# Kernel optimization log

Measured on AMD Instinct MI355X. Metric: run time of the kernel, lower is better.

## Reference

```python
import jax, jax.numpy as jnp
import numpy as np

N, E, D, H = 50000, 800000, 128, 64


def _norm_adj(edge_index, num_nodes):
    # add self loops, then w_ij = d_i^{-1/2} d_j^{-1/2} with deg = in-degree of col
    loops = jnp.arange(num_nodes)
    row = jnp.concatenate([edge_index[0], loops])
    col = jnp.concatenate([edge_index[1], loops])
    deg = jax.ops.segment_sum(jnp.ones_like(col, dtype=jnp.float32), col, num_segments=num_nodes)
    dinv = jnp.where(deg > 0, jax.lax.rsqrt(deg), 0.0)
    w = dinv[row] * dinv[col]
    return row, col, w


def _spmm(row, col, w, x, num_nodes):
    # y[row] += w * x[col]  (torch.sparse.mm(adj, x))
    return jax.ops.segment_sum(w[:, None] * x[col], row, num_segments=num_nodes)


def setup_inputs() -> dict:
    key = jax.random.key(0)
    ks = jax.random.split(key, 8)
    inp = {
        "x": jax.random.normal(ks[0], (N, D), dtype=jnp.float32),
        "edge_index": jax.random.randint(ks[1], (2, E), 0, N),
        "num_nodes": N,
    }
    # per-branch, per-layer Linear weights stored as [in, hid] (x @ W)
    wk = jax.random.split(ks[2], 6)
    s = 0.05
    inp["homo_W0"] = jax.random.normal(wk[0], (D, H), dtype=jnp.float32) * s
    inp["homo_W1"] = jax.random.normal(wk[1], (H, H), dtype=jnp.float32) * s
    inp["full_W0"] = jax.random.normal(wk[2], (D, H), dtype=jnp.float32) * s
    inp["full_W1"] = jax.random.normal(wk[3], (H, H), dtype=jnp.float32) * s
    inp["het_W0"] = jax.random.normal(wk[4], (D, H), dtype=jnp.float32) * s
    inp["het_W1"] = jax.random.normal(wk[5], (H, H), dtype=jnp.float32) * s
    for name in ("homo_a0", "homo_a1", "full_a0", "full_a1", "het_a0", "het_a1",
                 "w_homo", "w_full", "w_hetero"):
        inp[name] = jnp.float32(1.0)
    return inp


def reference(x, edge_index, num_nodes,
              homo_W0, homo_W1, full_W0, full_W1, het_W0, het_W1,
              homo_a0, homo_a1, full_a0, full_a1, het_a0, het_a1,
              w_homo, w_full, w_hetero):
    row, col, w = _norm_adj(edge_index, num_nodes)

    def homo_layer(h, W, a):
        return jax.nn.relu(a * (_spmm(row, col, w, h, num_nodes) @ W))

    def full_layer(h, W, a):
        return jax.nn.relu(a * (h @ W))

    def het_layer(h, W, a):
        # L = I - A  =>  L @ h = h - A @ h
        return jax.nn.relu(a * ((h - _spmm(row, col, w, h, num_nodes)) @ W))

    h_homo = homo_layer(homo_layer(x, homo_W0, homo_a0), homo_W1, homo_a1)
    h_full = full_layer(full_layer(x, full_W0, full_a0), full_W1, full_a1)
    h_het = het_layer(het_layer(x, het_W0, het_a0), het_W1, het_a1)
    combined = w_homo * h_homo + w_full * h_full + w_hetero * h_het
    return (combined, h_homo, h_full, h_het)
```

## Files before the change

### kernel.cpp

```cpp
#include <hip/hip_runtime.h>


typedef __attribute__((ext_vector_type(8))) short short8;
typedef __attribute__((ext_vector_type(4))) float f32x4;

static __device__ __forceinline__ unsigned short f2bf(float f) {
    unsigned int u = __float_as_uint(f);
    u += 0x7FFFu + ((u >> 16) & 1u);
    return (unsigned short)(u >> 16);
}
static __device__ __forceinline__ float bflo(unsigned int pv) {
    return __uint_as_float(pv << 16);
}
static __device__ __forceinline__ float bfhi(unsigned int pv) {
    return __uint_as_float(pv & 0xFFFF0000u);
}

#define PSHIFT 7
#define PSIZE  128
#define NPART_MAX 400
#define PCAP   3072
#define ACHUNK 6272

__global__ __launch_bounds__(256) void wpackT_kernel(
    const float* __restrict__ w10, const float* __restrict__ w11,
    const float* __restrict__ w12, const float* __restrict__ w20,
    const float* __restrict__ w21, const float* __restrict__ w22,
    unsigned short* __restrict__ out)
{
    const int i = blockIdx.x * 256 + threadIdx.x;
    const int L1 = 3 * 64 * 128;
    if (i < L1) {
        const int b = i >> 13, col = (i >> 7) & 63, k = i & 127;
        const float* __restrict__ w = (b == 0) ? w10 : ((b == 1) ? w11 : w12);
        out[i] = f2bf(w[k * 64 + col]);
    } else if (i < L1 + 3 * 64 * 64) {
        const int j = i - L1;
        const int b = j >> 12, col = (j >> 6) & 63, k = j & 63;
        const float* __restrict__ w = (b == 0) ? w20 : ((b == 1) ? w21 : w22);
        out[i] = f2bf(w[k * 64 + col]);
    }
}

__global__ __launch_bounds__(256) void radix_kernel(
    const int* __restrict__ ei, int E, int npart,
    int* __restrict__ gcnt_r, int* __restrict__ gcnt_c,
    unsigned int* __restrict__ rbuf, unsigned short* __restrict__ cbuf)
{
    __shared__ int hist_r[NPART_MAX], lofs_r[NPART_MAX], resv_r[NPART_MAX];
    __shared__ int hist_c[NPART_MAX], lofs_c[NPART_MAX], resv_c[NPART_MAX];
    __shared__ int seg_r[16], seg_c[16];
    __shared__ unsigned int   sr[ACHUNK];
    __shared__ unsigned short sc[ACHUNK];
    const int tid = threadIdx.x;
    const int e0 = blockIdx.x * ACHUNK;
    const int e1 = (e0 + ACHUNK < E) ? e0 + ACHUNK : E;
    const int cnt = e1 - e0;
    if (cnt <= 0) return;

    for (int i = tid; i < npart; i += 256) { hist_r[i] = 0; hist_c[i] = 0; }
    __syncthreads();

    for (int e = e0 + tid; e < e1; e += 256) {
        const int r = ei[e], c = ei[E + e];
        atomicAdd(&hist_r[r >> PSHIFT], 1);
        atomicAdd(&hist_c[c >> PSHIFT], 1);
    }
    __syncthreads();

    const int SEG = (npart + 7) / 8;
    if (tid < 8) {
        int s = 0;
        const int a = tid * SEG, b = (a + SEG < npart) ? a + SEG : npart;
        for (int i = a; i < b; ++i) { lofs_r[i] = s; s += hist_r[i]; }
        seg_r[tid] = s;
    } else if (tid >= 64 && tid < 72) {
        const int t = tid - 64;
        int s = 0;
        const int a = t * SEG, b = (a + SEG < npart) ? a + SEG : npart;
        for (int i = a; i < b; ++i) { lofs_c[i] = s; s += hist_c[i]; }
        seg_c[t] = s;
    }
    __syncthreads();
    if (tid == 0) {
        int s = 0;
        for (int k = 0; k < 8; ++k) { const int t = seg_r[k]; seg_r[k] = s; s += t; }
    } else if (tid == 64) {
        int s = 0;
        for (int k = 0; k < 8; ++k) { const int t = seg_c[k]; seg_c[k] = s; s += t; }
    }
    __syncthreads();
    for (int i = tid; i < npart; i += 256) {
        lofs_r[i] += seg_r[i / SEG];
        lofs_c[i] += seg_c[i / SEG];
    }
    __syncthreads();

    for (int i = tid; i < npart; i += 256) {
        resv_r[i] = atomicAdd(&gcnt_r[i], hist_r[i]);
        resv_c[i] = atomicAdd(&gcnt_c[i], hist_c[i]);
        hist_r[i] = 0; hist_c[i] = 0;
    }
    __syncthreads();

    for (int e = e0 + tid; e < e1; e += 256) {
        const int r = ei[e], c = ei[E + e];
        const int pr = r >> PSHIFT, pc = c >> PSHIFT;
        const int jr = lofs_r[pr] + atomicAdd(&hist_r[pr], 1);
        const int jc = lofs_c[pc] + atomicAdd(&hist_c[pc], 1);
        sr[jr] = ((unsigned int)r << 16) | (unsigned int)c;
        sc[jc] = (unsigned short)c;
    }
    __syncthreads();

    for (int j = tid; j < cnt; j += 256) {
        const unsigned int rc = sr[j];
        const int p = (int)(rc >> 16) >> PSHIFT;
        const int idx = resv_r[p] + (j - lofs_r[p]);
        if (idx < PCAP) rbuf[(size_t)p * PCAP + idx] = rc;
    }
    for (int j = tid; j < cnt; j += 256) {
        const unsigned short cv = sc[j];
        const int p = (int)cv >> PSHIFT;
        const int idx = resv_c[p] + (j - lofs_c[p]);
        if (idx < PCAP) cbuf[(size_t)p * PCAP + idx] = cv;
    }
}

__global__ __launch_bounds__(256) void bucket_kernel(
    const unsigned int* __restrict__ rbuf, const unsigned short* __restrict__ cbuf,
    const int* __restrict__ gcnt_r, const int* __restrict__ gcnt_c, int N,
    unsigned short* __restrict__ bucket, int* __restrict__ cur,
    float* __restrict__ dinv)
{
    __shared__ unsigned short sbucket[PSIZE * 64];
    __shared__ int scur[PSIZE], sdeg[PSIZE];
    const int tid = threadIdx.x;
    const int p = blockIdx.x;
    const int lo = p << PSHIFT;
    const int sl = (lo + PSIZE < N) ? PSIZE : N - lo;
    if (sl <= 0) return;

    for (int i = tid; i < sl; i += 256) { scur[i] = 0; sdeg[i] = 0; }
    __syncthreads();

    int cnt_r = gcnt_r[p]; if (cnt_r > PCAP) cnt_r = PCAP;
    int cnt_c = gcnt_c[p]; if (cnt_c > PCAP) cnt_c = PCAP;

    for (int e = tid; e < cnt_r; e += 256) {
        const unsigned int rc = rbuf[(size_t)p * PCAP + e];
        const int local = (int)(rc >> 16) - lo;
        const int pos = atomicAdd(&scur[local], 1);
        if (pos < 64) sbucket[local * 64 + pos] = (unsigned short)(rc & 0xFFFFu);
    }
    for (int e = tid; e < cnt_c; e += 256) {
        atomicAdd(&sdeg[(int)cbuf[(size_t)p * PCAP + e] - lo], 1);
    }
    __syncthreads();

    for (int i = tid; i < sl; i += 256) {
        cur[lo + i]  = scur[i];
        dinv[lo + i] = 1.0f / sqrtf((float)sdeg[i] + 1.0f);
    }
    unsigned int* gb = (unsigned int*)(bucket + (size_t)lo * 64);
    const unsigned int* sb = (const unsigned int*)sbucket;
    for (int i = tid; i < sl * 32; i += 256) gb[i] = sb[i];
}

__global__ __launch_bounds__(256) void gemm_l1_kernel(
    const float* __restrict__ x, const unsigned short* __restrict__ Wt,
    const float* __restrict__ dinv,
    unsigned short* __restrict__ Pb, unsigned short* __restrict__ full1b,
    const float* __restrict__ alphaF, int N)
{
    __shared__ __align__(16) unsigned short sx[64 * 136];
    const int tid = threadIdx.x;
    const int row0 = blockIdx.x * 64;

    #pragma unroll
    for (int j = 0; j < 8; ++j) {
        const int idx = j * 256 + tid;
        const int row = idx >> 5;
        const int c4  = idx & 31;
        float4 v = make_float4(0.f, 0.f, 0.f, 0.f);
        if (row0 + row < N) v = ((const float4*)x)[(size_t)(row0 + row) * 32 + c4];
        const unsigned int lo = (unsigned int)f2bf(v.x) | ((unsigned int)f2bf(v.y) << 16);
        const unsigned int hi = (unsigned int)f2bf(v.z) | ((unsigned int)f2bf(v.w) << 16);
        *(uint2*)&sx[row * 136 + c4 * 4] = make_uint2(lo, hi);
    }
    __syncthreads();

    const int lane = tid & 63;
    const int w = tid >> 6;
    const int g = lane >> 4;
    const int m = lane & 15;
    const float alpha = alphaF[0];

    short8 afr[4];
    #pragma unroll
    for (int kk = 0; kk < 4; ++kk)
        afr[kk] = *(const short8*)&sx[(16 * w + m) * 136 + kk * 32 + g * 8];

    const int rbase = row0 + 16 * w + g * 4;
    float dv[4];
    #pragma unroll
    for (int j = 0; j < 4; ++j)
        dv[j] = (rbase + j < N) ? dinv[rbase + j] : 0.f;

    #pragma unroll 1
    for (int b = 0; b < 3; ++b) {
        const unsigned short* __restrict__ Wb = Wt + b * 8192;
        f32x4 acc0 = {0.f, 0.f, 0.f, 0.f};
        f32x4 acc1 = {0.f, 0.f, 0.f, 0.f};
        f32x4 acc2 = {0.f, 0.f, 0.f, 0.f};
        f32x4 acc3 = {0.f, 0.f, 0.f, 0.f};
        #pragma unroll
        for (int kk = 0; kk < 4; ++kk) {
            const unsigned short* wk = Wb + m * 128 + kk * 32 + g * 8;
            const short8 b0 = *(const short8*)(wk);
            const short8 b1 = *(const short8*)(wk + 16 * 128);
            const short8 b2 = *(const short8*)(wk + 32 * 128);
            const short8 b3 = *(const short8*)(wk + 48 * 128);
            acc0 = __builtin_amdgcn_mfma_f32_16x16x32_bf16(afr[kk], b0, acc0, 0, 0, 0);
            acc1 = __builtin_amdgcn_mfma_f32_16x16x32_bf16(afr[kk], b1, acc1, 0, 0, 0);
            acc2 = __builtin_amdgcn_mfma_f32_16x16x32_bf16(afr[kk], b2, acc2, 0, 0, 0);
            acc3 = __builtin_amdgcn_mfma_f32_16x16x32_bf16(afr[kk], b3, acc3, 0, 0, 0);
        }
        #pragma unroll
        for (int j = 0; j < 4; ++j) {
            const int row = rbase + j;
            if (row < N) {
                if (b < 2) {
                    unsigned short* p = Pb + (size_t)row * 128 + b * 64 + m;
                    p[0]  = f2bf(dv[j] * acc0[j]);
                    p[16] = f2bf(dv[j] * acc1[j]);
                    p[32] = f2bf(dv[j] * acc2[j]);
                    p[48] = f2bf(dv[j] * acc3[j]);
                } else {
                    unsigned short* p = full1b + (size_t)row * 64 + m;
                    p[0]  = f2bf(fmaxf(alpha * acc0[j], 0.f));
                    p[16] = f2bf(fmaxf(alpha * acc1[j], 0.f));
                    p[32] = f2bf(fmaxf(alpha * acc2[j], 0.f));
                    p[48] = f2bf(fmaxf(alpha * acc3[j], 0.f));
                }
            }
        }
    }
}

__global__ __launch_bounds__(256) void gemm_l2_kernel(
    const unsigned short* __restrict__ h1b, const unsigned short* __restrict__ t1b,
    const unsigned short* __restrict__ f1b, const unsigned short* __restrict__ Wt2,
    const float* __restrict__ dinv,
    unsigned short* __restrict__ Qb, float* __restrict__ outF,
    const float* __restrict__ alphaF, int N)
{
    __shared__ __align__(16) unsigned short sx[3][64 * 72];
    const int tid = threadIdx.x;
    const int row0 = blockIdx.x * 64;

    #pragma unroll
    for (int b = 0; b < 3; ++b) {
        const unsigned short* __restrict__ in = (b == 0) ? h1b : ((b == 1) ? t1b : f1b);
        #pragma unroll
        for (int j = 0; j < 2; ++j) {
            const int idx = j * 256 + tid;
            const int row = idx >> 3, seg = idx & 7;
            uint4 v = make_uint4(0, 0, 0, 0);
            if (row0 + row < N) v = ((const uint4*)in)[(size_t)(row0 + row) * 8 + seg];
            *(uint4*)&sx[b][row * 72 + seg * 8] = v;
        }
    }
    __syncthreads();

    const int lane = tid & 63;
    const int w = tid >> 6;
    const int g = lane >> 4, m = lane & 15;
    const float alpha = alphaF[0];
    const int rbase = row0 + 16 * w + g * 4;

    float dv[4];
    #pragma unroll
    for (int j = 0; j < 4; ++j)
        dv[j] = (rbase + j < N) ? dinv[rbase + j] : 0.f;

    #pragma unroll 1
    for (int b = 0; b < 3; ++b) {
        const short8 afr0 = *(const short8*)&sx[b][(16 * w + m) * 72 + g * 8];
        const short8 afr1 = *(const short8*)&sx[b][(16 * w + m) * 72 + 32 + g * 8];
        const unsigned short* __restrict__ Wb = Wt2 + b * 4096;
        f32x4 acc0 = {0.f, 0.f, 0.f, 0.f};
        f32x4 acc1 = {0.f, 0.f, 0.f, 0.f};
        f32x4 acc2 = {0.f, 0.f, 0.f, 0.f};
        f32x4 acc3 = {0.f, 0.f, 0.f, 0.f};
        #pragma unroll
        for (int kk = 0; kk < 2; ++kk) {
            const short8 af = kk ? afr1 : afr0;
            const unsigned short* wk = Wb + m * 64 + kk * 32 + g * 8;
            const short8 b0 = *(const short8*)(wk);
            const short8 b1 = *(const short8*)(wk + 16 * 64);
            const short8 b2 = *(const short8*)(wk + 32 * 64);
            const short8 b3 = *(const short8*)(wk + 48 * 64);
            acc0 = __builtin_amdgcn_mfma_f32_16x16x32_bf16(af, b0, acc0, 0, 0, 0);
            acc1 = __builtin_amdgcn_mfma_f32_16x16x32_bf16(af, b1, acc1, 0, 0, 0);
            acc2 = __builtin_amdgcn_mfma_f32_16x16x32_bf16(af, b2, acc2, 0, 0, 0);
            acc3 = __builtin_amdgcn_mfma_f32_16x16x32_bf16(af, b3, acc3, 0, 0, 0);
        }
        #pragma unroll
        for (int j = 0; j < 4; ++j) {
            const int row = rbase + j;
            if (row < N) {
                if (b < 2) {
                    unsigned short* p = Qb + (size_t)row * 128 + b * 64 + m;
                    p[0]  = f2bf(dv[j] * acc0[j]);
                    p[16] = f2bf(dv[j] * acc1[j]);
                    p[32] = f2bf(dv[j] * acc2[j]);
                    p[48] = f2bf(dv[j] * acc3[j]);
                } else {
                    float* p = outF + (size_t)row * 64 + m;
                    p[0]  = fmaxf(alpha * acc0[j], 0.f);
                    p[16] = fmaxf(alpha * acc1[j], 0.f);
                    p[32] = fmaxf(alpha * acc2[j], 0.f);
                    p[48] = fmaxf(alpha * acc3[j], 0.f);
                }
            }
        }
    }
}

__global__ __launch_bounds__(256) void spmm1_kernel(
    const unsigned short* __restrict__ Pb, const unsigned short* __restrict__ bucket,
    const int* __restrict__ cnt, const float* __restrict__ dinv,
    unsigned short* __restrict__ homo1b, unsigned short* __restrict__ het1b,
    const float* __restrict__ aH, const float* __restrict__ aT, int N)
{
    const int i = blockIdx.x * 4 + (threadIdx.x >> 6);
    if (i >= N) return;
    const int lane = threadIdx.x & 63;
    const int g  = lane >> 4;
    const int fl = lane & 15;
    const uint4* __restrict__ P16 = (const uint4*)Pb;
    const float di = dinv[i];
    const uint4 us = P16[(size_t)i * 16 + fl];
    float ps[8];
    ps[0] = bflo(us.x); ps[1] = bfhi(us.x); ps[2] = bflo(us.y); ps[3] = bfhi(us.y);
    ps[4] = bflo(us.z); ps[5] = bfhi(us.z); ps[6] = bflo(us.w); ps[7] = bfhi(us.w);
    int n = cnt[i]; if (n > 64) n = 64;
    const unsigned int* __restrict__ bp = (const unsigned int*)(bucket + (size_t)i * 64);
    float acc[8];
    #pragma unroll
    for (int j = 0; j < 8; ++j) acc[j] = 0.f;

    for (int k0 = 0; k0 < n; k0 += 16) {
        const int wbase = (k0 >> 1) + (g >> 1);
        const unsigned int pw0 = bp[wbase];
        const unsigned int pw1 = bp[wbase + 2];
        const unsigned int pw2 = bp[wbase + 4];
        const unsigned int pw3 = bp[wbase + 6];
        const int k_0 = k0 + g, k_1 = k0 + 4 + g, k_2 = k0 + 8 + g, k_3 = k0 + 12 + g;
        const int c0 = (k_0 < n) ? (int)((g & 1) ? (pw0 >> 16) : (pw0 & 0xFFFFu)) : i;
        const int c1 = (k_1 < n) ? (int)((g & 1) ? (pw1 >> 16) : (pw1 & 0xFFFFu)) : i;
        const int c2 = (k_2 < n) ? (int)((g & 1) ? (pw2 >> 16) : (pw2 & 0xFFFFu)) : i;
        const int c3 = (k_3 < n) ? (int)((g & 1) ? (pw3 >> 16) : (pw3 & 0xFFFFu)) : i;
        const float s0 = (k_0 < n) ? 1.f : 0.f;
        const float s1 = (k_1 < n) ? 1.f : 0.f;
        const float s2 = (k_2 < n) ? 1.f : 0.f;
        const float s3 = (k_3 < n) ? 1.f : 0.f;
        const uint4 u0 = P16[(size_t)c0 * 16 + fl];
        const uint4 u1 = P16[(size_t)c1 * 16 + fl];
        const uint4 u2 = P16[(size_t)c2 * 16 + fl];
        const uint4 u3 = P16[(size_t)c3 * 16 + fl];
        acc[0] = fmaf(s0, bflo(u0.x), acc[0]); acc[1] = fmaf(s0, bfhi(u0.x), acc[1]);
        acc[2] = fmaf(s0, bflo(u0.y), acc[2]); acc[3] = fmaf(s0, bfhi(u0.y), acc[3]);
        acc[4] = fmaf(s0, bflo(u0.z), acc[4]); acc[5] = fmaf(s0, bfhi(u0.z), acc[5]);
        acc[6] = fmaf(s0, bflo(u0.w), acc[6]); acc[7] = fmaf(s0, bfhi(u0.w), acc[7]);
        acc[0] = fmaf(s1, bflo(u1.x), acc[0]); acc[1] = fmaf(s1, bfhi(u1.x), acc[1]);
        acc[2] = fmaf(s1, bflo(u1.y), acc[2]); acc[3] = fmaf(s1, bfhi(u1.y), acc[3]);
        acc[4] = fmaf(s1, bflo(u1.z), acc[4]); acc[5] = fmaf(s1, bfhi(u1.z), acc[5]);
        acc[6] = fmaf(s1, bflo(u1.w), acc[6]); acc[7] = fmaf(s1, bfhi(u1.w), acc[7]);
        acc[0] = fmaf(s2, bflo(u2.x), acc[0]); acc[1] = fmaf(s2, bfhi(u2.x), acc[1]);
        acc[2] = fmaf(s2, bflo(u2.y), acc[2]); acc[3] = fmaf(s2, bfhi(u2.y), acc[3]);
        acc[4] = fmaf(s2, bflo(u2.z), acc[4]); acc[5] = fmaf(s2, bfhi(u2.z), acc[5]);
        acc[6] = fmaf(s2, bflo(u2.w), acc[6]); acc[7] = fmaf(s2, bfhi(u2.w), acc[7]);
        acc[0] = fmaf(s3, bflo(u3.x), acc[0]); acc[1] = fmaf(s3, bfhi(u3.x), acc[1]);
        acc[2] = fmaf(s3, bflo(u3.y), acc[2]); acc[3] = fmaf(s3, bfhi(u3.y), acc[3]);
        acc[4] = fmaf(s3, bflo(u3.z), acc[4]); acc[5] = fmaf(s3, bfhi(u3.z), acc[5]);
        acc[6] = fmaf(s3, bflo(u3.w), acc[6]); acc[7] = fmaf(s3, bfhi(u3.w), acc[7]);
    }
    float y[8];
    #pragma unroll
    for (int j = 0; j < 8; ++j) {
        acc[j] += __shfl_xor(acc[j], 16);
        acc[j] += __shfl_xor(acc[j], 32);
        y[j] = di * (acc[j] + ps[j]);
    }
    if (lane < 8) {
        const float a = aH[0];
        uint4 o;
        o.x = (unsigned int)f2bf(fmaxf(a * y[0], 0.f)) |
              ((unsigned int)f2bf(fmaxf(a * y[1], 0.f)) << 16);
        o.y = (unsigned int)f2bf(fmaxf(a * y[2], 0.f)) |
              ((unsigned int)f2bf(fmaxf(a * y[3], 0.f)) << 16);
        o.z = (unsigned int)f2bf(fmaxf(a * y[4], 0.f)) |
              ((unsigned int)f2bf(fmaxf(a * y[5], 0.f)) << 16);
        o.w = (unsigned int)f2bf(fmaxf(a * y[6], 0.f)) |
              ((unsigned int)f2bf(fmaxf(a * y[7], 0.f)) << 16);
        ((uint4*)homo1b)[(size_t)i * 8 + lane] = o;
    } else if (lane < 16) {
        const float a = aT[0];
        const float rdi = 1.0f / di;
        float v[8];
        #pragma unroll
        for (int j = 0; j < 8; ++j) v[j] = fmaxf(a * (ps[j] * rdi - y[j]), 0.f);
        uint4 o;
        o.x = (unsigned int)f2bf(v[0]) | ((unsigned int)f2bf(v[1]) << 16);
        o.y = (unsigned int)f2bf(v[2]) | ((unsigned int)f2bf(v[3]) << 16);
        o.z = (unsigned int)f2bf(v[4]) | ((unsigned int)f2bf(v[5]) << 16);
        o.w = (unsigned int)f2bf(v[6]) | ((unsigned int)f2bf(v[7]) << 16);
        ((uint4*)het1b)[(size_t)i * 8 + (lane - 8)] = o;
    }
}

__global__ __launch_bounds__(256) void spmm2_kernel(
    const unsigned short* __restrict__ Qb, const unsigned short* __restrict__ bucket,
    const int* __restrict__ cnt, const float* __restrict__ dinv,
    const float* __restrict__ full2,
    float* __restrict__ outComb, float* __restrict__ outHomo, float* __restrict__ outHet,
    const float* __restrict__ aH, const float* __restrict__ aT,
    const float* __restrict__ wH, const float* __restrict__ wF, const float* __restrict__ wT,
    int N)
{
    const int i = blockIdx.x * 4 + (threadIdx.x >> 6);
    if (i >= N) return;
    const int lane = threadIdx.x & 63;
    const int g  = lane >> 4;
    const int fl = lane & 15;
    const uint4* __restrict__ Q16 = (const uint4*)Qb;
    const float di = dinv[i];
    const uint4 us = Q16[(size_t)i * 16 + fl];
    float ps[8];
    ps[0] = bflo(us.x); ps[1] = bfhi(us.x); ps[2] = bflo(us.y); ps[3] = bfhi(us.y);
    ps[4] = bflo(us.z); ps[5] = bfhi(us.z); ps[6] = bflo(us.w); ps[7] = bfhi(us.w);
    int n = cnt[i]; if (n > 64) n = 64;
    const unsigned int* __restrict__ bp = (const unsigned int*)(bucket + (size_t)i * 64);
    float acc[8];
    #pragma unroll
    for (int j = 0; j < 8; ++j) acc[j] = 0.f;

    for (int k0 = 0; k0 < n; k0 += 16) {
        const int wbase = (k0 >> 1) + (g >> 1);
        const unsigned int pw0 = bp[wbase];
        const unsigned int pw1 = bp[wbase + 2];
        const unsigned int pw2 = bp[wbase + 4];
        const unsigned int pw3 = bp[wbase + 6];
        const int k_0 = k0 + g, k_1 = k0 + 4 + g, k_2 = k0 + 8 + g, k_3 = k0 + 12 + g;
        const int c0 = (k_0 < n) ? (int)((g & 1) ? (pw0 >> 16) : (pw0 & 0xFFFFu)) : i;
        const int c1 = (k_1 < n) ? (int)((g & 1) ? (pw1 >> 16) : (pw1 & 0xFFFFu)) : i;
        const int c2 = (k_2 < n) ? (int)((g & 1) ? (pw2 >> 16) : (pw2 & 0xFFFFu)) : i;
        const int c3 = (k_3 < n) ? (int)((g & 1) ? (pw3 >> 16) : (pw3 & 0xFFFFu)) : i;
        const float s0 = (k_0 < n) ? 1.f : 0.f;
        const float s1 = (k_1 < n) ? 1.f : 0.f;
        const float s2 = (k_2 < n) ? 1.f : 0.f;
        const float s3 = (k_3 < n) ? 1.f : 0.f;
        const uint4 u0 = Q16[(size_t)c0 * 16 + fl];
        const uint4 u1 = Q16[(size_t)c1 * 16 + fl];
        const uint4 u2 = Q16[(size_t)c2 * 16 + fl];
        const uint4 u3 = Q16[(size_t)c3 * 16 + fl];
        acc[0] = fmaf(s0, bflo(u0.x), acc[0]); acc[1] = fmaf(s0, bfhi(u0.x), acc[1]);
        acc[2] = fmaf(s0, bflo(u0.y), acc[2]); acc[3] = fmaf(s0, bfhi(u0.y), acc[3]);
        acc[4] = fmaf(s0, bflo(u0.z), acc[4]); acc[5] = fmaf(s0, bfhi(u0.z), acc[5]);
        acc[6] = fmaf(s0, bflo(u0.w), acc[6]); acc[7] = fmaf(s0, bfhi(u0.w), acc[7]);
        acc[0] = fmaf(s1, bflo(u1.x), acc[0]); acc[1] = fmaf(s1, bfhi(u1.x), acc[1]);
        acc[2] = fmaf(s1, bflo(u1.y), acc[2]); acc[3] = fmaf(s1, bfhi(u1.y), acc[3]);
        acc[4] = fmaf(s1, bflo(u1.z), acc[4]); acc[5] = fmaf(s1, bfhi(u1.z), acc[5]);
        acc[6] = fmaf(s1, bflo(u1.w), acc[6]); acc[7] = fmaf(s1, bfhi(u1.w), acc[7]);
        acc[0] = fmaf(s2, bflo(u2.x), acc[0]); acc[1] = fmaf(s2, bfhi(u2.x), acc[1]);
        acc[2] = fmaf(s2, bflo(u2.y), acc[2]); acc[3] = fmaf(s2, bfhi(u2.y), acc[3]);
        acc[4] = fmaf(s2, bflo(u2.z), acc[4]); acc[5] = fmaf(s2, bfhi(u2.z), acc[5]);
        acc[6] = fmaf(s2, bflo(u2.w), acc[6]); acc[7] = fmaf(s2, bfhi(u2.w), acc[7]);
        acc[0] = fmaf(s3, bflo(u3.x), acc[0]); acc[1] = fmaf(s3, bfhi(u3.x), acc[1]);
        acc[2] = fmaf(s3, bflo(u3.y), acc[2]); acc[3] = fmaf(s3, bfhi(u3.y), acc[3]);
        acc[4] = fmaf(s3, bflo(u3.z), acc[4]); acc[5] = fmaf(s3, bfhi(u3.z), acc[5]);
        acc[6] = fmaf(s3, bflo(u3.w), acc[6]); acc[7] = fmaf(s3, bfhi(u3.w), acc[7]);
    }
    float y[8];
    #pragma unroll
    for (int j = 0; j < 8; ++j) {
        acc[j] += __shfl_xor(acc[j], 16);
        acc[j] += __shfl_xor(acc[j], 32);
        y[j] = di * (acc[j] + ps[j]);
    }
    float v[8];
    if (fl < 8) {
        const float a = aH[0];
        #pragma unroll
        for (int j = 0; j < 8; ++j) v[j] = fmaxf(a * y[j], 0.f);
    } else {
        const float a = aT[0];
        const float rdi = 1.0f / di;
        #pragma unroll
        for (int j = 0; j < 8; ++j) v[j] = fmaxf(a * (ps[j] * rdi - y[j]), 0.f);
    }
    if (lane < 8) {
        float4* dst = (float4*)(outHomo + (size_t)i * 64 + 8 * lane);
        dst[0] = make_float4(v[0], v[1], v[2], v[3]);
        dst[1] = make_float4(v[4], v[5], v[6], v[7]);
    } else if (lane < 16) {
        float4* dst = (float4*)(outHet + (size_t)i * 64 + 8 * (lane - 8));
        dst[0] = make_float4(v[0], v[1], v[2], v[3]);
        dst[1] = make_float4(v[4], v[5], v[6], v[7]);
    }
    float t[8];
    #pragma unroll
    for (int j = 0; j < 8; ++j) t[j] = __shfl_xor(v[j], 8);
    if (lane < 8) {
        const float4* f4 = (const float4*)(full2 + (size_t)i * 64 + 8 * lane);
        const float4 fa = f4[0], fb = f4[1];
        const float cwh = wH[0], cwf = wF[0], cwt = wT[0];
        float4* dst = (float4*)(outComb + (size_t)i * 64 + 8 * lane);
        dst[0] = make_float4(cwh * v[0] + cwf * fa.x + cwt * t[0],
                             cwh * v[1] + cwf * fa.y + cwt * t[1],
                             cwh * v[2] + cwf * fa.z + cwt * t[2],
                             cwh * v[3] + cwf * fa.w + cwt * t[3]);
        dst[1] = make_float4(cwh * v[4] + cwf * fb.x + cwt * t[4],
                             cwh * v[5] + cwf * fb.y + cwt * t[5],
                             cwh * v[6] + cwf * fb.z + cwt * t[6],
                             cwh * v[7] + cwf * fb.w + cwt * t[7]);
    }
}

extern "C" void kernel_launch(void* const* d_in, const int* in_sizes, int n_in,
                              void* d_out, int out_size, void* d_ws, size_t ws_size,
                              hipStream_t stream)
{
    const float* x  = (const float*)d_in[0];
    const int*   ei = (const int*)d_in[1];
    const int N = in_sizes[0] / 128;
    const int E = in_sizes[1] / 2;
    const float* homo_W0 = (const float*)d_in[3];
    const float* homo_W1 = (const float*)d_in[4];
    const float* full_W0 = (const float*)d_in[5];
    const float* full_W1 = (const float*)d_in[6];
    const float* het_W0  = (const float*)d_in[7];
    const float* het_W1  = (const float*)d_in[8];
    const float* homo_a0 = (const float*)d_in[9];
    const float* homo_a1 = (const float*)d_in[10];
    const float* full_a0 = (const float*)d_in[11];
    const float* full_a1 = (const float*)d_in[12];
    const float* het_a0  = (const float*)d_in[13];
    const float* het_a1  = (const float*)d_in[14];
    const float* w_homo  = (const float*)d_in[15];
    const float* w_full  = (const float*)d_in[16];
    const float* w_het   = (const float*)d_in[17];

    char* ws = (char*)d_ws;
    size_t off = 0;
    auto alloc = [&](size_t bytes) -> char* {
        char* p = ws + off;
        off = (off + bytes + 511) & ~(size_t)511;
        return p;
    };
    int*            cur    = (int*)alloc((size_t)N * 4);
    float*          dinv   = (float*)alloc((size_t)N * 4);
    unsigned short* bucket = (unsigned short*)alloc((size_t)N * 64 * 2);
    int*            gcnt   = (int*)alloc((size_t)2 * NPART_MAX * 4);
    unsigned short* Wt     = (unsigned short*)alloc((size_t)(3 * 64 * 128 + 3 * 64 * 64) * 2);
    const size_t rbuf_sz = (size_t)NPART_MAX * PCAP * 4;
    const size_t cbuf_sz = (size_t)NPART_MAX * PCAP * 2;
    size_t unionA_sz = (size_t)N * 128 * 2;
    if (rbuf_sz + cbuf_sz > unionA_sz) unionA_sz = rbuf_sz + cbuf_sz;
    char*           unionA = alloc(unionA_sz);
    unsigned int*   rbuf   = (unsigned int*)unionA;
    unsigned short* cbuf   = (unsigned short*)(unionA + rbuf_sz);
    unsigned short* Pb     = (unsigned short*)unionA;
    unsigned short* full1b = (unsigned short*)alloc((size_t)N * 64 * 2);
    unsigned short* homo1b = (unsigned short*)alloc((size_t)N * 64 * 2);
    unsigned short* het1b  = (unsigned short*)alloc((size_t)N * 64 * 2);
    unsigned short* Qb     = Pb;

    float* out      = (float*)d_out;
    float* outComb  = out;
    float* outHomo  = out + (size_t)N * 64;
    float* outFull  = out + (size_t)2 * N * 64;
    float* outHet   = out + (size_t)3 * N * 64;

    const int npart = (N + PSIZE - 1) >> PSHIFT;

    hipMemsetAsync(gcnt, 0, (size_t)2 * NPART_MAX * 4, stream);

    wpackT_kernel<<<(3 * 64 * 128 + 3 * 64 * 64 + 255) / 256, 256, 0, stream>>>(
        homo_W0, het_W0, full_W0, homo_W1, het_W1, full_W1, Wt);

    const int ablocks = (E + ACHUNK - 1) / ACHUNK;
    radix_kernel<<<ablocks, 256, 0, stream>>>(
        ei, E, npart, gcnt, gcnt + NPART_MAX, rbuf, cbuf);
    bucket_kernel<<<npart, 256, 0, stream>>>(
        rbuf, cbuf, gcnt, gcnt + NPART_MAX, N, bucket, cur, dinv);

    gemm_l1_kernel<<<(N + 63) / 64, 256, 0, stream>>>(
        x, Wt, dinv, Pb, full1b, full_a0, N);
    spmm1_kernel<<<(N + 3) / 4, 256, 0, stream>>>(
        Pb, bucket, cur, dinv, homo1b, het1b, homo_a0, het_a0, N);

    gemm_l2_kernel<<<(N + 63) / 64, 256, 0, stream>>>(
        homo1b, het1b, full1b, Wt + 3 * 64 * 128, dinv, Qb, outFull, full_a1, N);
    spmm2_kernel<<<(N + 3) / 4, 256, 0, stream>>>(
        Qb, bucket, cur, dinv, outFull, outComb, outHomo, outHet,
        homo_a1, het_a1, w_homo, w_full, w_het, N);
}
```

Measured before the change: 159.7 us.

## Split radix partitioning by side, fuse counter reset, vectorize bucket loads

```diff
diff --git a/kernel.cpp b/kernel.cpp
--- a/kernel.cpp
+++ b/kernel.cpp
@@ -20,15 +20,16 @@
 #define PSIZE  128
 #define NPART_MAX 400
 #define PCAP   3072
-#define ACHUNK 6272
-
-__global__ __launch_bounds__(256) void wpackT_kernel(
+#define ACHUNK 3136
+
+__global__ __launch_bounds__(256) void prep_kernel(
     const float* __restrict__ w10, const float* __restrict__ w11,
     const float* __restrict__ w12, const float* __restrict__ w20,
     const float* __restrict__ w21, const float* __restrict__ w22,
-    unsigned short* __restrict__ out)
+    unsigned short* __restrict__ out, int* __restrict__ gcnt)
 {
     const int i = blockIdx.x * 256 + threadIdx.x;
+    if (i < 2 * NPART_MAX) gcnt[i] = 0;
     const int L1 = 3 * 64 * 128;
     if (i < L1) {
         const int b = i >> 13, col = (i >> 7) & 63, k = i & 127;
@@ -47,83 +48,77 @@
     int* __restrict__ gcnt_r, int* __restrict__ gcnt_c,
     unsigned int* __restrict__ rbuf, unsigned short* __restrict__ cbuf)
 {
-    __shared__ int hist_r[NPART_MAX], lofs_r[NPART_MAX], resv_r[NPART_MAX];
-    __shared__ int hist_c[NPART_MAX], lofs_c[NPART_MAX], resv_c[NPART_MAX];
-    __shared__ int seg_r[16], seg_c[16];
-    __shared__ unsigned int   sr[ACHUNK];
-    __shared__ unsigned short sc[ACHUNK];
+    __shared__ int hist[NPART_MAX], lofs[NPART_MAX], resv[NPART_MAX];
+    __shared__ int seg[8];
+    __shared__ unsigned int sbuf[ACHUNK];
+    const int side  = blockIdx.x & 1;
+    const int chunk = blockIdx.x >> 1;
     const int tid = threadIdx.x;
-    const int e0 = blockIdx.x * ACHUNK;
+    const int e0 = chunk * ACHUNK;
     const int e1 = (e0 + ACHUNK < E) ? e0 + ACHUNK : E;
     const int cnt = e1 - e0;
     if (cnt <= 0) return;
-
-    for (int i = tid; i < npart; i += 256) { hist_r[i] = 0; hist_c[i] = 0; }
-    __syncthreads();
-
-    for (int e = e0 + tid; e < e1; e += 256) {
-        const int r = ei[e], c = ei[E + e];
-        atomicAdd(&hist_r[r >> PSHIFT], 1);
-        atomicAdd(&hist_c[c >> PSHIFT], 1);
-    }
+    const int* __restrict__ keys = side ? (ei + E) : ei;
+
+    for (int i = tid; i < npart; i += 256) hist[i] = 0;
+    __syncthreads();
+
+    for (int e = e0 + tid; e < e1; e += 256)
+        atomicAdd(&hist[keys[e] >> PSHIFT], 1);
     __syncthreads();
 
     const int SEG = (npart + 7) / 8;
     if (tid < 8) {
         int s = 0;
         const int a = tid * SEG, b = (a + SEG < npart) ? a + SEG : npart;
-        for (int i = a; i < b; ++i) { lofs_r[i] = s; s += hist_r[i]; }
-        seg_r[tid] = s;
-    } else if (tid >= 64 && tid < 72) {
-        const int t = tid - 64;
-        int s = 0;
-        const int a = t * SEG, b = (a + SEG < npart) ? a + SEG : npart;
-        for (int i = a; i < b; ++i) { lofs_c[i] = s; s += hist_c[i]; }
-        seg_c[t] = s;
+        for (int i = a; i < b; ++i) { lofs[i] = s; s += hist[i]; }
+        seg[tid] = s;
     }
     __syncthreads();
     if (tid == 0) {
         int s = 0;
-        for (int k = 0; k < 8; ++k) { const int t = seg_r[k]; seg_r[k] = s; s += t; }
-    } else if (tid == 64) {
-        int s = 0;
-        for (int k = 0; k < 8; ++k) { const int t = seg_c[k]; seg_c[k] = s; s += t; }
-    }
-    __syncthreads();
+        for (int k = 0; k < 8; ++k) { const int t = seg[k]; seg[k] = s; s += t; }
+    }
+    __syncthreads();
+    for (int i = tid; i < npart; i += 256) lofs[i] += seg[i / SEG];
+    __syncthreads();
+
+    int* __restrict__ gcnt = side ? gcnt_c : gcnt_r;
     for (int i = tid; i < npart; i += 256) {
-        lofs_r[i] += seg_r[i / SEG];
-        lofs_c[i] += seg_c[i / SEG];
-    }
-    __syncthreads();
-
-    for (int i = tid; i < npart; i += 256) {
-        resv_r[i] = atomicAdd(&gcnt_r[i], hist_r[i]);
-        resv_c[i] = atomicAdd(&gcnt_c[i], hist_c[i]);
-        hist_r[i] = 0; hist_c[i] = 0;
-    }
-    __syncthreads();
-
-    for (int e = e0 + tid; e < e1; e += 256) {
-        const int r = ei[e], c = ei[E + e];
-        const int pr = r >> PSHIFT, pc = c >> PSHIFT;
-        const int jr = lofs_r[pr] + atomicAdd(&hist_r[pr], 1);
-        const int jc = lofs_c[pc] + atomicAdd(&hist_c[pc], 1);
-        sr[jr] = ((unsigned int)r << 16) | (unsigned int)c;
-        sc[jc] = (unsigned short)c;
-    }
-    __syncthreads();
-
-    for (int j = tid; j < cnt; j += 256) {
-        const unsigned int rc = sr[j];
-        const int p = (int)(rc >> 16) >> PSHIFT;
-        const int idx = resv_r[p] + (j - lofs_r[p]);
-        if (idx < PCAP) rbuf[(size_t)p * PCAP + idx] = rc;
-    }
-    for (int j = tid; j < cnt; j += 256) {
-        const unsigned short cv = sc[j];
-        const int p = (int)cv >> PSHIFT;
-        const int idx = resv_c[p] + (j - lofs_c[p]);
-        if (idx < PCAP) cbuf[(size_t)p * PCAP + idx] = cv;
+        resv[i] = atomicAdd(&gcnt[i], hist[i]);
+        hist[i] = 0;
+    }
+    __syncthreads();
+
+    if (side == 0) {
+        for (int e = e0 + tid; e < e1; e += 256) {
+            const int r = ei[e], c = ei[E + e];
+            const int p = r >> PSHIFT;
+            const int j = lofs[p] + atomicAdd(&hist[p], 1);
+            sbuf[j] = ((unsigned int)r << 16) | (unsigned int)c;
+        }
+        __syncthreads();
+        for (int j = tid; j < cnt; j += 256) {
+            const unsigned int rc = sbuf[j];
+            const int p = (int)(rc >> 16) >> PSHIFT;
+            const int idx = resv[p] + (j - lofs[p]);
+            if (idx < PCAP) rbuf[(size_t)p * PCAP + idx] = rc;
+        }
+    } else {
+        unsigned short* sc = (unsigned short*)sbuf;
+        for (int e = e0 + tid; e < e1; e += 256) {
+            const int c = ei[E + e];
+            const int p = c >> PSHIFT;
+            const int j = lofs[p] + atomicAdd(&hist[p], 1);
+            sc[j] = (unsigned short)c;
+        }
+        __syncthreads();
+        for (int j = tid; j < cnt; j += 256) {
+            const unsigned short cv = sc[j];
+            const int p = (int)cv >> PSHIFT;
+            const int idx = resv[p] + (j - lofs[p]);
+            if (idx < PCAP) cbuf[(size_t)p * PCAP + idx] = cv;
+        }
     }
 }
 
@@ -339,6 +334,7 @@
     const int lane = threadIdx.x & 63;
     const int g  = lane >> 4;
     const int fl = lane & 15;
+    const int gh = g & 1;
     const uint4* __restrict__ P16 = (const uint4*)Pb;
     const float di = dinv[i];
     const uint4 us = P16[(size_t)i * 16 + fl];
@@ -346,26 +342,22 @@
     ps[0] = bflo(us.x); ps[1] = bfhi(us.x); ps[2] = bflo(us.y); ps[3] = bfhi(us.y);
     ps[4] = bflo(us.z); ps[5] = bfhi(us.z); ps[6] = bflo(us.w); ps[7] = bfhi(us.w);
     int n = cnt[i]; if (n > 64) n = 64;
-    const unsigned int* __restrict__ bp = (const unsigned int*)(bucket + (size_t)i * 64);
+    const uint4* __restrict__ bp4 = (const uint4*)(bucket + (size_t)i * 64);
     float acc[8];
     #pragma unroll
     for (int j = 0; j < 8; ++j) acc[j] = 0.f;
 
     for (int k0 = 0; k0 < n; k0 += 16) {
-        const int wbase = (k0 >> 1) + (g >> 1);
-        const unsigned int pw0 = bp[wbase];
-        const unsigned int pw1 = bp[wbase + 2];
-        const unsigned int pw2 = bp[wbase + 4];
-        const unsigned int pw3 = bp[wbase + 6];
-        const int k_0 = k0 + g, k_1 = k0 + 4 + g, k_2 = k0 + 8 + g, k_3 = k0 + 12 + g;
-        const int c0 = (k_0 < n) ? (int)((g & 1) ? (pw0 >> 16) : (pw0 & 0xFFFFu)) : i;
-        const int c1 = (k_1 < n) ? (int)((g & 1) ? (pw1 >> 16) : (pw1 & 0xFFFFu)) : i;
-        const int c2 = (k_2 < n) ? (int)((g & 1) ? (pw2 >> 16) : (pw2 & 0xFFFFu)) : i;
-        const int c3 = (k_3 < n) ? (int)((g & 1) ? (pw3 >> 16) : (pw3 & 0xFFFFu)) : i;
-        const float s0 = (k_0 < n) ? 1.f : 0.f;
-        const float s1 = (k_1 < n) ? 1.f : 0.f;
-        const float s2 = (k_2 < n) ? 1.f : 0.f;
-        const float s3 = (k_3 < n) ? 1.f : 0.f;
+        const uint4 w4 = bp4[(k0 >> 3) + (g >> 1)];
+        const int kb = k0 + 8 * (g >> 1) + gh;
+        const int c0 = (kb     < n) ? (int)(gh ? (w4.x >> 16) : (w4.x & 0xFFFFu)) : i;
+        const int c1 = (kb + 2 < n) ? (int)(gh ? (w4.y >> 16) : (w4.y & 0xFFFFu)) : i;
+        const int c2 = (kb + 4 < n) ? (int)(gh ? (w4.z >> 16) : (w4.z & 0xFFFFu)) : i;
+        const int c3 = (kb + 6 < n) ? (int)(gh ? (w4.w >> 16) : (w4.w & 0xFFFFu)) : i;
+        const float s0 = (kb     < n) ? 1.f : 0.f;
+        const float s1 = (kb + 2 < n) ? 1.f : 0.f;
+        const float s2 = (kb + 4 < n) ? 1.f : 0.f;
+        const float s3 = (kb + 6 < n) ? 1.f : 0.f;
         const uint4 u0 = P16[(size_t)c0 * 16 + fl];
         const uint4 u1 = P16[(size_t)c1 * 16 + fl];
         const uint4 u2 = P16[(size_t)c2 * 16 + fl];
@@ -435,6 +427,7 @@
     const int lane = threadIdx.x & 63;
     const int g  = lane >> 4;
     const int fl = lane & 15;
+    const int gh = g & 1;
     const uint4* __restrict__ Q16 = (const uint4*)Qb;
     const float di = dinv[i];
     const uint4 us = Q16[(size_t)i * 16 + fl];
@@ -442,26 +435,22 @@
     ps[0] = bflo(us.x); ps[1] = bfhi(us.x); ps[2] = bflo(us.y); ps[3] = bfhi(us.y);
     ps[4] = bflo(us.z); ps[5] = bfhi(us.z); ps[6] = bflo(us.w); ps[7] = bfhi(us.w);
     int n = cnt[i]; if (n > 64) n = 64;
-    const unsigned int* __restrict__ bp = (const unsigned int*)(bucket + (size_t)i * 64);
+    const uint4* __restrict__ bp4 = (const uint4*)(bucket + (size_t)i * 64);
     float acc[8];
     #pragma unroll
     for (int j = 0; j < 8; ++j) acc[j] = 0.f;
 
     for (int k0 = 0; k0 < n; k0 += 16) {
-        const int wbase = (k0 >> 1) + (g >> 1);
-        const unsigned int pw0 = bp[wbase];
-        const unsigned int pw1 = bp[wbase + 2];
-        const unsigned int pw2 = bp[wbase + 4];
-        const unsigned int pw3 = bp[wbase + 6];
-        const int k_0 = k0 + g, k_1 = k0 + 4 + g, k_2 = k0 + 8 + g, k_3 = k0 + 12 + g;
-        const int c0 = (k_0 < n) ? (int)((g & 1) ? (pw0 >> 16) : (pw0 & 0xFFFFu)) : i;
-        const int c1 = (k_1 < n) ? (int)((g & 1) ? (pw1 >> 16) : (pw1 & 0xFFFFu)) : i;
-        const int c2 = (k_2 < n) ? (int)((g & 1) ? (pw2 >> 16) : (pw2 & 0xFFFFu)) : i;
-        const int c3 = (k_3 < n) ? (int)((g & 1) ? (pw3 >> 16) : (pw3 & 0xFFFFu)) : i;
-        const float s0 = (k_0 < n) ? 1.f : 0.f;
-        const float s1 = (k_1 < n) ? 1.f : 0.f;
-        const float s2 = (k_2 < n) ? 1.f : 0.f;
-        const float s3 = (k_3 < n) ? 1.f : 0.f;
+        const uint4 w4 = bp4[(k0 >> 3) + (g >> 1)];
+        const int kb = k0 + 8 * (g >> 1) + gh;
+        const int c0 = (kb     < n) ? (int)(gh ? (w4.x >> 16) : (w4.x & 0xFFFFu)) : i;
+        const int c1 = (kb + 2 < n) ? (int)(gh ? (w4.y >> 16) : (w4.y & 0xFFFFu)) : i;
+        const int c2 = (kb + 4 < n) ? (int)(gh ? (w4.z >> 16) : (w4.z & 0xFFFFu)) : i;
+        const int c3 = (kb + 6 < n) ? (int)(gh ? (w4.w >> 16) : (w4.w & 0xFFFFu)) : i;
+        const float s0 = (kb     < n) ? 1.f : 0.f;
+        const float s1 = (kb + 2 < n) ? 1.f : 0.f;
+        const float s2 = (kb + 4 < n) ? 1.f : 0.f;
+        const float s3 = (kb + 6 < n) ? 1.f : 0.f;
         const uint4 u0 = Q16[(size_t)c0 * 16 + fl];
         const uint4 u1 = Q16[(size_t)c1 * 16 + fl];
         const uint4 u2 = Q16[(size_t)c2 * 16 + fl];
@@ -586,13 +575,11 @@
 
     const int npart = (N + PSIZE - 1) >> PSHIFT;
 
-    hipMemsetAsync(gcnt, 0, (size_t)2 * NPART_MAX * 4, stream);
-
-    wpackT_kernel<<<(3 * 64 * 128 + 3 * 64 * 64 + 255) / 256, 256, 0, stream>>>(
-        homo_W0, het_W0, full_W0, homo_W1, het_W1, full_W1, Wt);
-
-    const int ablocks = (E + ACHUNK - 1) / ACHUNK;
-    radix_kernel<<<ablocks, 256, 0, stream>>>(
+    prep_kernel<<<(3 * 64 * 128 + 3 * 64 * 64 + 255) / 256, 256, 0, stream>>>(
+        homo_W0, het_W0, full_W0, homo_W1, het_W1, full_W1, Wt, gcnt);
+
+    const int nchunks = (E + ACHUNK - 1) / ACHUNK;
+    radix_kernel<<<2 * nchunks, 256, 0, stream>>>(
         ei, E, npart, gcnt, gcnt + NPART_MAX, rbuf, cbuf);
     bucket_kernel<<<npart, 256, 0, stream>>>(
         rbuf, cbuf, gcnt, gcnt + NPART_MAX, N, bucket, cur, dinv);
```

New measurement: 151.5 us. 5.2% less time.
